# Optimization experiments

Hardware: AMD Instinct MI355X
Metric: run time of the kernel (lower is better)

## Reference

```python
import jax, jax.numpy as jnp
import numpy as np

B, M, T, D, V = 16, 1024, 4096, 512, 32000
HOPS = 2  # multi_layer_gcn layer_number=2


def setup_inputs() -> dict:
    key = jax.random.key(0)
    ks = jax.random.split(key, 10)
    s = 1.0 / np.sqrt(D)
    emb = jax.random.normal(ks[0], (V, D), jnp.float32) * 0.02
    Ws = jax.random.normal(ks[1], (HOPS, D, D), jnp.float32) * s
    Wn = jax.random.normal(ks[2], (HOPS, D, D), jnp.float32) * s
    Wr = jax.random.normal(ks[3], (HOPS, D, D), jnp.float32) * s
    Wt = jax.random.normal(ks[4], (D, 3 * D), jnp.float32) * (1.0 / np.sqrt(3 * D))
    concept_ids = jax.random.randint(ks[5], (B, M), 0, V)
    relation = jax.random.randint(ks[6], (B, T), 0, V)
    head = jax.random.randint(ks[7], (B, T), 0, M)
    tail = jax.random.randint(ks[8], (B, T), 0, M)
    triple_label = jax.random.randint(ks[9], (B, T), -1, 2)  # {-1,0,1}
    return dict(emb=emb, Ws=Ws, Wn=Wn, Wr=Wr, Wt=Wt,
                concept_ids=concept_ids, relation=relation,
                head=head, tail=tail, triple_label=triple_label)


def _forward(emb, Ws, Wn, Wr, Wt, concept_ids, relation, head, tail, triple_label):
    x = emb[concept_ids]        # [B, M, D] node hidden
    rel = emb[relation]         # [B, T, D] relation hidden
    mask = (triple_label != -1).astype(x.dtype)  # [B, T]

    # per-batch scatter_add into M node slots
    scat = jax.vmap(lambda msg, idx: jnp.zeros((M, msg.shape[-1]), msg.dtype).at[idx].add(msg))
    scat1 = jax.vmap(lambda v, idx: jnp.zeros((M,), v.dtype).at[idx].add(v))

    for i in range(HOPS):
        oh = jnp.take_along_axis(x, head[..., None], axis=1) * mask[..., None]  # gather heads
        ot = jnp.take_along_axis(x, tail[..., None], axis=1) * mask[..., None]  # gather tails
        relm = rel * mask[..., None]
        # update_node += scatter(head_repr - rel -> tail) + scatter(tail_repr - rel -> head)
        upd = scat(oh - relm, tail) + scat(ot - relm, head)          # [B, M, D]
        cnt = scat1(mask, tail) + scat1(mask, head)                  # [B, M]
        x = jax.nn.relu(
            jnp.einsum('bmd,ed->bme', x, Ws[i])
            + jnp.einsum('bmd,ed->bme', upd, Wn[i]) / jnp.maximum(cnt, 1.0)[..., None]
        )
        rel = jnp.einsum('btd,ed->bte', rel, Wr[i])

    head_repr = jnp.take_along_axis(x, head[..., None], axis=1)  # [B, T, D]
    tail_repr = jnp.take_along_axis(x, tail[..., None], axis=1)  # [B, T, D]
    triple_repr = jnp.concatenate([head_repr, rel, tail_repr], axis=-1)  # [B, T, 3D]
    triple_repr = jnp.einsum('btk,dk->btd', triple_repr, Wt)     # [B, T, D]
    encoded_cause = triple_repr.sum(axis=1)                      # [B, D]
    return triple_repr, encoded_cause


def reference(emb, Ws, Wn, Wr, Wt, concept_ids, relation, head, tail, triple_label):
    return _forward(emb, Ws, Wn, Wr, Wt, concept_ids, relation, head, tail, triple_label)
```

## Files before the change

kernel.cpp:

```cpp
#include <hip/hip_runtime.h>

namespace {

constexpr int kB = 16;
constexpr int kM = 1024;
constexpr int kT = 4096;
constexpr int kD = 512;
constexpr int kV = 32000;

typedef __attribute__((ext_vector_type(8))) short bfrag8;
typedef __attribute__((ext_vector_type(4))) float f4acc;

__device__ __forceinline__ ushort f2bf(float f) {
  unsigned u = __float_as_uint(f);
  u += 0x7fffu + ((u >> 16) & 1u);
  return (ushort)(u >> 16);
}
__device__ __forceinline__ float bf2f(ushort h) {
  return __uint_as_float(((unsigned)h) << 16);
}

__device__ __forceinline__ void gload_lds16(const void* g, void* l) {
  __builtin_amdgcn_global_load_lds(
      (const __attribute__((address_space(1))) void*)g,
      (__attribute__((address_space(3))) void*)l, 16, 0, 0);
}

constexpr int kN0 = kV * kD / 4;
constexpr int kN1 = kN0 + 2 * kD * kD / 4;
constexpr int kN2 = kN1 + 2 * kD * kD / 4;
constexpr int kN3 = kN2 + kD * 1536 / 4;
constexpr int kN4 = kN3 + kB * kM * 128;
constexpr int kPREPB = kN4 / 8192;
constexpr int kCSRB = 16;
constexpr int kMM2B = 256;

__global__ __launch_bounds__(512) void fused_prep_k(
    const float4* __restrict__ emb, const float4* __restrict__ Ws,
    const float4* __restrict__ Wn, const float4* __restrict__ Wt,
    const float* __restrict__ Wnf, const float* __restrict__ Wtf,
    const float* __restrict__ Wrf,
    const int* __restrict__ cid,
    const int* __restrict__ headp, const int* __restrict__ tailp,
    const int* __restrict__ lblp,
    ushort4* __restrict__ EMBb, ushort4* __restrict__ Wsb,
    ushort4* __restrict__ Wnb, ushort4* __restrict__ Wtb,
    ushort4* __restrict__ X0,
    int* __restrict__ deg, int* __restrict__ rowstart, int* __restrict__ epack,
    ushort* __restrict__ Wn2r, float* __restrict__ T1)
{
  __shared__ __align__(16) char shm[45056];
  const int bid = blockIdx.x;
  const int tid = threadIdx.x;

  if (bid < kCSRB) {
    int* sdeg = (int*)shm;
    int* sscan = (int*)(shm + 4096);
    int* sfill = (int*)(shm + 8192);
    int* sep = (int*)(shm + 12288);
    const int b = bid;
    const int n0 = tid, n1 = tid + 512;
    sdeg[n0] = 0; sdeg[n1] = 0;
    __syncthreads();
    const int* hb = headp + (b << 12);
    const int* tb = tailp + (b << 12);
    const int* lb = lblp + (b << 12);
    for (int t = tid; t < kT; t += 512) {
      if (lb[t] == -1) continue;
      atomicAdd(&sdeg[tb[t]], 1);
      atomicAdd(&sdeg[hb[t]], 1);
    }
    __syncthreads();
    int d0 = sdeg[n0], d1 = sdeg[n1];
    sscan[n0] = d0; sscan[n1] = d1;
    __syncthreads();
    for (int off = 1; off < kM; off <<= 1) {
      int v0 = (n0 >= off) ? sscan[n0 - off] : 0;
      int v1 = (n1 >= off) ? sscan[n1 - off] : 0;
      __syncthreads();
      sscan[n0] += v0; sscan[n1] += v1;
      __syncthreads();
    }
    int lrs0 = sscan[n0] - d0;
    int lrs1 = sscan[n1] - d1;
    deg[(b << 10) + n0] = d0;
    deg[(b << 10) + n1] = d1;
    rowstart[(b << 10) + n0] = b * (2 * kT) + lrs0;
    rowstart[(b << 10) + n1] = b * (2 * kT) + lrs1;
    sfill[n0] = lrs0; sfill[n1] = lrs1;
    __syncthreads();
    for (int t = tid; t < kT; t += 512) {
      if (lb[t] == -1) continue;
      int hd = hb[t];
      int tl = tb[t];
      int p0 = atomicAdd(&sfill[tl], 1);
      sep[p0] = ((t * 2) << 10) | hd;
      int p1 = atomicAdd(&sfill[hd], 1);
      sep[p1] = ((t * 2 + 1) << 10) | tl;
    }
    __syncthreads();
#pragma unroll
    for (int nn = 0; nn < 2; ++nn) {
      int lrs = nn ? lrs1 : lrs0;
      int d = nn ? d1 : d0;
      for (int i = 1; i < d; ++i) {
        int key = sep[lrs + i];
        int j = i - 1;
        while (j >= 0 && sep[lrs + j] > key) {
          sep[lrs + j + 1] = sep[lrs + j];
          --j;
        }
        sep[lrs + j + 1] = key;
      }
    }
    __syncthreads();
    for (int i = tid; i < 2 * kT; i += 512)
      epack[b * (2 * kT) + i] = sep[i];
  } else if (bid < kCSRB + kPREPB) {
    const int bidp = bid - kCSRB;
    for (int c = 0; c < 4; ++c) {
      const int base = (bidp * 4 + c) * 2048 + tid;
      const float4* sp[4];
      ushort4* dp[4];
#pragma unroll
      for (int j = 0; j < 4; ++j) {
        int i = base + j * 512;
        if (i < kN0) { sp[j] = emb + i; dp[j] = EMBb + i; }
        else if (i < kN1) { sp[j] = Ws + (i - kN0); dp[j] = Wsb + (i - kN0); }
        else if (i < kN2) { sp[j] = Wn + (i - kN1); dp[j] = Wnb + (i - kN1); }
        else if (i < kN3) { sp[j] = Wt + (i - kN2); dp[j] = Wtb + (i - kN2); }
        else {
          int idx = i - kN3;
          sp[j] = emb + (size_t)cid[idx >> 7] * 128 + (idx & 127);
          dp[j] = X0 + idx;
        }
      }
      float4 v[4];
#pragma unroll
      for (int j = 0; j < 4; ++j) v[j] = *sp[j];
#pragma unroll
      for (int j = 0; j < 4; ++j) {
        ushort4 o;
        o.x = f2bf(v[j].x); o.y = f2bf(v[j].y);
        o.z = f2bf(v[j].z); o.w = f2bf(v[j].w);
        *dp[j] = o;
      }
    }
  } else {
    float (*prow)[512] = (float(*)[512])shm;
    const int mb = bid - kCSRB - kPREPB;
    const int job = mb >> 7;
    const int e0 = (mb & 127) * 4;
    const int k = tid;
    const float* P;
    int strideP, offsP;
    const float* Q;
    if (job == 0) { P = Wnf + (size_t)kD * kD; strideP = 512; offsP = 0; Q = Wrf; }
    else { P = Wtf; strideP = 1536; offsP = 512; Q = Wrf + (size_t)kD * kD; }
#pragma unroll
    for (int i = 0; i < 4; ++i)
      prow[i][k] = P[(size_t)(e0 + i) * strideP + offsP + k];
    __syncthreads();
    float acc[4] = {0.f, 0.f, 0.f, 0.f};
    for (int a = 0; a < 512; a += 8) {
      float qv[8];
#pragma unroll
      for (int u = 0; u < 8; ++u) qv[u] = Q[(a + u) * 512 + k];
#pragma unroll
      for (int u = 0; u < 8; ++u)
#pragma unroll
        for (int i = 0; i < 4; ++i)
          acc[i] = fmaf(prow[i][a + u], qv[u], acc[i]);
    }
#pragma unroll
    for (int i = 0; i < 4; ++i) {
      if (job == 0) Wn2r[(e0 + i) * 512 + k] = f2bf(acc[i]);
      else T1[(e0 + i) * 512 + k] = acc[i];
    }
  }
}

constexpr int kFOLDB = 128;

__global__ __launch_bounds__(512) void fold_aggxr_k(
    const float* __restrict__ T1, const float* __restrict__ Wrf,
    ushort* __restrict__ Wfold,
    const ushort4* __restrict__ Xv, const ushort4* __restrict__ EMBv,
    const int* __restrict__ relid,
    const int* __restrict__ deg, const int* __restrict__ rowstart,
    const int* __restrict__ epack,
    ushort4* __restrict__ SxC, ushort4* __restrict__ nSr0n)
{
  __shared__ float prow[4][512];
  const int bid = blockIdx.x;
  const int tid = threadIdx.x;
  if (bid < kFOLDB) {
    int e0 = bid * 4;
    int k = tid;
#pragma unroll
    for (int i = 0; i < 4; ++i)
      prow[i][k] = T1[(size_t)(e0 + i) * 512 + k];
    __syncthreads();
    float acc[4] = {0.f, 0.f, 0.f, 0.f};
    for (int a = 0; a < 512; a += 8) {
      float qv[8];
#pragma unroll
      for (int u = 0; u < 8; ++u) qv[u] = Wrf[(a + u) * 512 + k];
#pragma unroll
      for (int u = 0; u < 8; ++u)
#pragma unroll
        for (int i = 0; i < 4; ++i)
          acc[i] = fmaf(prow[i][a + u], qv[u], acc[i]);
    }
#pragma unroll
    for (int i = 0; i < 4; ++i) Wfold[(e0 + i) * 512 + k] = f2bf(acc[i]);
  } else {
    int bm = (bid - kFOLDB) * 4 + (tid >> 7);
    int t128 = tid & 127;
    int b = bm >> 10;
    int dg = deg[bm];
    int rs = rowstart[bm];
    const int* rid = relid + (b << 12);
    size_t xbase = (size_t)b * kM * 128;
    float ax = 0.f, ay = 0.f, az = 0.f, aw = 0.f;
    float rx = 0.f, ry = 0.f, rz = 0.f, rw = 0.f;
    int e = 0;
    for (; e + 4 <= dg; e += 4) {
      int pk[4];
#pragma unroll
      for (int j = 0; j < 4; ++j) pk[j] = epack[rs + e + j];
      ushort4 xv[4], rv[4];
#pragma unroll
      for (int j = 0; j < 4; ++j) {
        xv[j] = Xv[xbase + (size_t)(pk[j] & 1023) * 128 + t128];
        rv[j] = EMBv[(size_t)rid[pk[j] >> 11] * 128 + t128];
      }
#pragma unroll
      for (int j = 0; j < 4; ++j) {
        ax += bf2f(xv[j].x); ay += bf2f(xv[j].y);
        az += bf2f(xv[j].z); aw += bf2f(xv[j].w);
        rx += bf2f(rv[j].x); ry += bf2f(rv[j].y);
        rz += bf2f(rv[j].z); rw += bf2f(rv[j].w);
      }
    }
    for (; e < dg; ++e) {
      int pk = epack[rs + e];
      ushort4 xv = Xv[xbase + (size_t)(pk & 1023) * 128 + t128];
      ushort4 rv = EMBv[(size_t)rid[pk >> 11] * 128 + t128];
      ax += bf2f(xv.x); ay += bf2f(xv.y); az += bf2f(xv.z); aw += bf2f(xv.w);
      rx += bf2f(rv.x); ry += bf2f(rv.y); rz += bf2f(rv.z); rw += bf2f(rv.w);
    }
    float s = 1.0f / (float)(dg > 0 ? dg : 1);
    ushort4 o;
    o.x = f2bf((ax - rx) * s); o.y = f2bf((ay - ry) * s);
    o.z = f2bf((az - rz) * s); o.w = f2bf((aw - rw) * s);
    SxC[(size_t)bm * 128 + t128] = o;
    o.x = f2bf(-rx * s); o.y = f2bf(-ry * s);
    o.z = f2bf(-rz * s); o.w = f2bf(-rw * s);
    nSr0n[(size_t)bm * 128 + t128] = o;
  }
}

__global__ __launch_bounds__(128) void agg_x_k(
    const ushort4* __restrict__ Xv,
    const int* __restrict__ deg, const int* __restrict__ rowstart,
    const int* __restrict__ epack, ushort4* __restrict__ outv)
{
  int bm = blockIdx.x;
  int b = bm >> 10;
  int tid = threadIdx.x;
  int dg = deg[bm];
  int rs = rowstart[bm];
  size_t xbase = (size_t)b * kM * 128;
  float ax = 0.f, ay = 0.f, az = 0.f, aw = 0.f;
  int e = 0;
  for (; e + 4 <= dg; e += 4) {
    int pk[4];
#pragma unroll
    for (int j = 0; j < 4; ++j) pk[j] = epack[rs + e + j];
    ushort4 xv[4];
#pragma unroll
    for (int j = 0; j < 4; ++j)
      xv[j] = Xv[xbase + (size_t)(pk[j] & 1023) * 128 + tid];
#pragma unroll
    for (int j = 0; j < 4; ++j) {
      ax += bf2f(xv[j].x); ay += bf2f(xv[j].y);
      az += bf2f(xv[j].z); aw += bf2f(xv[j].w);
    }
  }
  for (; e < dg; ++e) {
    int src = epack[rs + e] & 1023;
    ushort4 xv = Xv[xbase + (size_t)src * 128 + tid];
    ax += bf2f(xv.x); ay += bf2f(xv.y); az += bf2f(xv.z); aw += bf2f(xv.w);
  }
  float s = 1.0f / (float)(dg > 0 ? dg : 1);
  ushort4 o;
  o.x = f2bf(ax * s); o.y = f2bf(ay * s); o.z = f2bf(az * s); o.w = f2bf(aw * s);
  outv[(size_t)bm * 128 + tid] = o;
}

template<int MODE>
__global__ __launch_bounds__(256) void gemm_k(
    const ushort* __restrict__ A0, const ushort* __restrict__ A1,
    const ushort* __restrict__ A2,
    const ushort* __restrict__ W1, const ushort* __restrict__ W2,
    const ushort* __restrict__ W3,
    ushort* __restrict__ outbf)
{
  constexpr int NSEG = (MODE == 0) ? 3 : (MODE == 1) ? 2 : 1;
  constexpr bool RELU = (MODE == 0) || (MODE == 1);
  constexpr int NC = (MODE == 4) ? 8 : 4;
  constexpr int OSTR = (MODE == 4) ? 1024 : 512;
  constexpr bool SWZ = (MODE != 5);

  __shared__ __align__(16) char lds[32768];
  char* ldsA = lds;
  char* ldsB = lds + 16384;
  const int tid = threadIdx.x;
  const int w = tid >> 6;
  const int l = tid & 63;
  const int wr = w >> 1;
  const int wc = w & 1;
  const int bid = blockIdx.x;
  int panel, col;
  if constexpr (SWZ) {
    int xcd = bid & 7;
    int idx = bid >> 3;
    panel = xcd * (((int)gridDim.x >> 3) / NC) + idx / NC;
    col = idx % NC;
  } else {
    panel = bid >> 2;
    col = bid & 3;
  }
  const int rowBase = panel * 128;
  const int colBase = col * 128;

  f4acc acc[4][4];
#pragma unroll
  for (int i = 0; i < 4; ++i)
#pragma unroll
    for (int j = 0; j < 4; ++j) acc[i][j] = (f4acc)(0.f);

  int lrow[4], gc[4];
#pragma unroll
  for (int i = 0; i < 4; ++i) {
    int P = (i * 4 + w) * 64 + l;
    lrow[i] = P >> 3;
    gc[i] = (P & 7) ^ (lrow[i] & 7);
  }

  for (int seg = 0; seg < NSEG; ++seg) {
    const char* aP[4];
    const char* bP[4];
#pragma unroll
    for (int i = 0; i < 4; ++i) {
      int grow = rowBase + lrow[i];
      const ushort* ab;
      if constexpr (MODE == 0) {
        ab = (seg == 0 ? A0 : (seg == 1 ? A1 : A2)) + (size_t)grow * kD;
      } else if constexpr (MODE == 1) {
        ab = (seg == 0 ? A0 : A1) + (size_t)grow * kD;
      } else {
        ab = A0 + (size_t)grow * kD;
      }
      aP[i] = (const char*)ab + gc[i] * 16;
      int e = colBase + lrow[i];
      const ushort* wb;
      if constexpr (MODE == 0) {
        wb = (seg == 0 ? W1 : (seg == 1 ? W2 : W3)) + (size_t)e * kD;
      } else if constexpr (MODE == 1) {
        wb = (seg == 0 ? W1 : W2) + (size_t)e * kD;
      } else if constexpr (MODE == 4) {
        wb = W1 + (size_t)(e & 511) * 1536 + (e >> 9) * 1024;
      } else {
        wb = W1 + (size_t)e * kD;
      }
      bP[i] = (const char*)wb + gc[i] * 16;
    }
    for (int kcl = 0; kcl < 8; ++kcl) {
      __syncthreads();
#pragma unroll
      for (int i = 0; i < 4; ++i) {
        gload_lds16(aP[i] + kcl * 128, ldsA + (i * 4 + w) * 1024);
        gload_lds16(bP[i] + kcl * 128, ldsB + (i * 4 + w) * 1024);
      }
      __syncthreads();
#pragma unroll
      for (int ksub = 0; ksub < 2; ++ksub) {
        bfrag8 ef[4], wf[4];
#pragma unroll
        for (int mi = 0; mi < 4; ++mi) {
          int r = wr * 64 + mi * 16 + (l & 15);
          int g = (ksub * 4 + (l >> 4)) ^ (r & 7);
          ef[mi] = *(const bfrag8*)(ldsA + r * 128 + g * 16);
        }
#pragma unroll
        for (int ni = 0; ni < 4; ++ni) {
          int e = wc * 64 + ni * 16 + (l & 15);
          int g = (ksub * 4 + (l >> 4)) ^ (e & 7);
          wf[ni] = *(const bfrag8*)(ldsB + e * 128 + g * 16);
        }
#pragma unroll
        for (int mi = 0; mi < 4; ++mi)
#pragma unroll
          for (int ni = 0; ni < 4; ++ni)
            acc[mi][ni] = __builtin_amdgcn_mfma_f32_16x16x32_bf16(
                wf[ni], ef[mi], acc[mi][ni], 0, 0, 0);
      }
    }
  }

#pragma unroll
  for (int mi = 0; mi < 4; ++mi) {
    int rr = rowBase + wr * 64 + mi * 16 + (l & 15);
#pragma unroll
    for (int ni = 0; ni < 4; ++ni) {
      int cc0 = colBase + wc * 64 + ni * 16 + (l >> 4) * 4;
      float v0 = acc[mi][ni][0], v1 = acc[mi][ni][1];
      float v2 = acc[mi][ni][2], v3 = acc[mi][ni][3];
      if constexpr (RELU) {
        v0 = fmaxf(v0, 0.f); v1 = fmaxf(v1, 0.f);
        v2 = fmaxf(v2, 0.f); v3 = fmaxf(v3, 0.f);
      }
      ushort4 o;
      o.x = f2bf(v0); o.y = f2bf(v1); o.z = f2bf(v2); o.w = f2bf(v3);
      *(ushort4*)(outbf + (size_t)rr * OSTR + cc0) = o;
    }
  }
}

__global__ __launch_bounds__(128) void final_add_k(
    const ushort4* __restrict__ REL2v, const ushort4* __restrict__ HTv,
    const int* __restrict__ relid, const int* __restrict__ headp,
    const int* __restrict__ tailp,
    float* __restrict__ outf, float* __restrict__ part)
{
  const int blk = blockIdx.x;
  const int tid = threadIdx.x;
  const int r0 = blk * 32;
  float cs0 = 0.f, cs1 = 0.f, cs2 = 0.f, cs3 = 0.f;
  for (int i = 0; i < 32; i += 8) {
    ushort4 rv[8], hv[8], tv[8];
#pragma unroll
    for (int j = 0; j < 8; ++j) {
      int r = r0 + i + j;
      int bb = r >> 12;
      rv[j] = REL2v[(size_t)relid[r] * 128 + tid];
      hv[j] = HTv[((size_t)(bb << 10) + headp[r]) * 256 + tid];
      tv[j] = HTv[((size_t)(bb << 10) + tailp[r]) * 256 + 128 + tid];
    }
#pragma unroll
    for (int j = 0; j < 8; ++j) {
      f4acc ov;
      ov[0] = bf2f(rv[j].x) + bf2f(hv[j].x) + bf2f(tv[j].x);
      ov[1] = bf2f(rv[j].y) + bf2f(hv[j].y) + bf2f(tv[j].y);
      ov[2] = bf2f(rv[j].z) + bf2f(hv[j].z) + bf2f(tv[j].z);
      ov[3] = bf2f(rv[j].w) + bf2f(hv[j].w) + bf2f(tv[j].w);
      cs0 += ov[0]; cs1 += ov[1]; cs2 += ov[2]; cs3 += ov[3];
      __builtin_nontemporal_store(
          ov, (f4acc*)(outf + (size_t)(r0 + i + j) * 512 + tid * 4));
    }
  }
  float4 o; o.x = cs0; o.y = cs1; o.z = cs2; o.w = cs3;
  *(float4*)(part + (size_t)blk * 512 + tid * 4) = o;
}

__global__ __launch_bounds__(512) void reduce_enc_k(
    const float* __restrict__ part, float* __restrict__ enc)
{
  int b = blockIdx.x;
  int c = threadIdx.x;
  float s = 0.f;
  for (int rt = 0; rt < 128; ++rt) s += part[(size_t)(b * 128 + rt) * 512 + c];
  enc[b * 512 + c] = s;
}

}

extern "C" void kernel_launch(void* const* d_in, const int* in_sizes, int n_in,
                              void* d_out, int out_size, void* d_ws, size_t ws_size,
                              hipStream_t stream) {
  const float* emb = (const float*)d_in[0];
  const float* Ws = (const float*)d_in[1];
  const float* Wn = (const float*)d_in[2];
  const float* Wr = (const float*)d_in[3];
  const float* Wt = (const float*)d_in[4];
  const int* cid = (const int*)d_in[5];
  const int* relid = (const int*)d_in[6];
  const int* headp = (const int*)d_in[7];
  const int* tailp = (const int*)d_in[8];
  const int* lblp = (const int*)d_in[9];
  float* out = (float*)d_out;

  char* wsp = (char*)d_ws;
  ushort* EMBb  = (ushort*)(wsp);
  ushort* HT    = (ushort*)(wsp);
  ushort* REL2  = (ushort*)(wsp + (32ull << 20));
  ushort* Wsb   = (ushort*)(wsp + (64ull << 20));
  ushort* Wnb   = (ushort*)(wsp + (65ull << 20));
  ushort* Wtb   = (ushort*)(wsp + (66ull << 20));
  ushort* Wn2r  = (ushort*)(wsp + (67ull << 20) + (512ull << 10));
  ushort* Wfold = (ushort*)(wsp + (68ull << 20));
  float*  T1    = (float*)(wsp + (68ull << 20) + (512ull << 10));
  int* deg      = (int*)(wsp + (70ull << 20));
  int* rowstart = deg + kB * kM;
  int* epack    = rowstart + kB * kM;
  float* part   = (float*)(wsp + (71ull << 20));

  char* outc = (char*)d_out;
  ushort* X0    = (ushort*)(outc);
  ushort* Sxn   = (ushort*)(outc + (16ull << 20));
  ushort* nSr0n = (ushort*)(outc + (32ull << 20));
  ushort* X1    = (ushort*)(outc + (48ull << 20));
  ushort* X2    = X0;
  float* ENC = out + (size_t)kB * kT * kD;

  fused_prep_k<<<kCSRB + kPREPB + kMM2B, 512, 0, stream>>>(
      (const float4*)emb, (const float4*)Ws, (const float4*)Wn,
      (const float4*)Wt, Wn, Wt, Wr, cid, headp, tailp, lblp,
      (ushort4*)EMBb, (ushort4*)Wsb, (ushort4*)Wnb, (ushort4*)Wtb,
      (ushort4*)X0, deg, rowstart, epack, Wn2r, T1);

  fold_aggxr_k<<<kFOLDB + kB * kM / 4, 512, 0, stream>>>(
      T1, Wr, Wfold, (const ushort4*)X0, (const ushort4*)EMBb, relid,
      deg, rowstart, epack, (ushort4*)Sxn, (ushort4*)nSr0n);

  gemm_k<1><<<(kB * kM / 128) * 4, 256, 0, stream>>>(
      X0, Sxn, nullptr, Wsb, Wnb, nullptr, X1);

  gemm_k<5><<<(kV / 128) * 4, 256, 0, stream>>>(
      EMBb, nullptr, nullptr, Wfold, nullptr, nullptr, REL2);

  agg_x_k<<<kB * kM, 128, 0, stream>>>(
      (const ushort4*)X1, deg, rowstart, epack, (ushort4*)Sxn);

  gemm_k<0><<<(kB * kM / 128) * 4, 256, 0, stream>>>(
      X1, Sxn, nSr0n, Wsb + (size_t)kD * kD, Wnb + (size_t)kD * kD, Wn2r, X2);

  gemm_k<4><<<(kB * kM / 128) * 8, 256, 0, stream>>>(
      X2, nullptr, nullptr, Wtb, nullptr, nullptr, HT);

  final_add_k<<<kB * kT / 32, 128, 0, stream>>>(
      (const ushort4*)REL2, (const ushort4*)HT, relid, headp, tailp, out, part);

  reduce_enc_k<<<kB, 512, 0, stream>>>(part, ENC);
}
```

Before: 261.4 us.

## Split per-batch CSR build into parallel count, scan, fill and sort kernels

Replaces the 16-block in-LDS CSR construction (degree count, scan, fill, insertion sort), which ran inside the prep kernel, with a pipeline. Degree counting now uses global atomics spread over 128 blocks, followed by separate scan, fill and per-row sort kernels. The aim is to stop 16 long-running blocks from serialising the prep kernel's tail. In exchange it adds a memset, three extra launches, and global-memory atomics and sorting in place of LDS.

```diff
diff --git a/kernel.cpp b/kernel.cpp
--- a/kernel.cpp
+++ b/kernel.cpp
@@ -31,8 +31,8 @@
 constexpr int kN2 = kN1 + 2 * kD * kD / 4;
 constexpr int kN3 = kN2 + kD * 1536 / 4;
 constexpr int kN4 = kN3 + kB * kM * 128;
+constexpr int kCNTB = 128;
 constexpr int kPREPB = kN4 / 8192;
-constexpr int kCSRB = 16;
 constexpr int kMM2B = 256;
 
 __global__ __launch_bounds__(512) void fused_prep_k(
@@ -46,78 +46,22 @@
     ushort4* __restrict__ EMBb, ushort4* __restrict__ Wsb,
     ushort4* __restrict__ Wnb, ushort4* __restrict__ Wtb,
     ushort4* __restrict__ X0,
-    int* __restrict__ deg, int* __restrict__ rowstart, int* __restrict__ epack,
+    int* __restrict__ deg,
     ushort* __restrict__ Wn2r, float* __restrict__ T1)
 {
-  __shared__ __align__(16) char shm[45056];
+  __shared__ __align__(16) float prow[4][512];
   const int bid = blockIdx.x;
   const int tid = threadIdx.x;
 
-  if (bid < kCSRB) {
-    int* sdeg = (int*)shm;
-    int* sscan = (int*)(shm + 4096);
-    int* sfill = (int*)(shm + 8192);
-    int* sep = (int*)(shm + 12288);
-    const int b = bid;
-    const int n0 = tid, n1 = tid + 512;
-    sdeg[n0] = 0; sdeg[n1] = 0;
-    __syncthreads();
-    const int* hb = headp + (b << 12);
-    const int* tb = tailp + (b << 12);
-    const int* lb = lblp + (b << 12);
-    for (int t = tid; t < kT; t += 512) {
-      if (lb[t] == -1) continue;
-      atomicAdd(&sdeg[tb[t]], 1);
-      atomicAdd(&sdeg[hb[t]], 1);
-    }
-    __syncthreads();
-    int d0 = sdeg[n0], d1 = sdeg[n1];
-    sscan[n0] = d0; sscan[n1] = d1;
-    __syncthreads();
-    for (int off = 1; off < kM; off <<= 1) {
-      int v0 = (n0 >= off) ? sscan[n0 - off] : 0;
-      int v1 = (n1 >= off) ? sscan[n1 - off] : 0;
-      __syncthreads();
-      sscan[n0] += v0; sscan[n1] += v1;
-      __syncthreads();
-    }
-    int lrs0 = sscan[n0] - d0;
-    int lrs1 = sscan[n1] - d1;
-    deg[(b << 10) + n0] = d0;
-    deg[(b << 10) + n1] = d1;
-    rowstart[(b << 10) + n0] = b * (2 * kT) + lrs0;
-    rowstart[(b << 10) + n1] = b * (2 * kT) + lrs1;
-    sfill[n0] = lrs0; sfill[n1] = lrs1;
-    __syncthreads();
-    for (int t = tid; t < kT; t += 512) {
-      if (lb[t] == -1) continue;
-      int hd = hb[t];
-      int tl = tb[t];
-      int p0 = atomicAdd(&sfill[tl], 1);
-      sep[p0] = ((t * 2) << 10) | hd;
-      int p1 = atomicAdd(&sfill[hd], 1);
-      sep[p1] = ((t * 2 + 1) << 10) | tl;
-    }
-    __syncthreads();
-#pragma unroll
-    for (int nn = 0; nn < 2; ++nn) {
-      int lrs = nn ? lrs1 : lrs0;
-      int d = nn ? d1 : d0;
-      for (int i = 1; i < d; ++i) {
-        int key = sep[lrs + i];
-        int j = i - 1;
-        while (j >= 0 && sep[lrs + j] > key) {
-          sep[lrs + j + 1] = sep[lrs + j];
-          --j;
-        }
-        sep[lrs + j + 1] = key;
-      }
-    }
-    __syncthreads();
-    for (int i = tid; i < 2 * kT; i += 512)
-      epack[b * (2 * kT) + i] = sep[i];
-  } else if (bid < kCSRB + kPREPB) {
-    const int bidp = bid - kCSRB;
+  if (bid < kCNTB) {
+    int i = bid * 512 + tid;
+    if (lblp[i] != -1) {
+      int b = i >> 12;
+      atomicAdd(&deg[(b << 10) + tailp[i]], 1);
+      atomicAdd(&deg[(b << 10) + headp[i]], 1);
+    }
+  } else if (bid < kCNTB + kPREPB) {
+    const int bidp = bid - kCNTB;
     for (int c = 0; c < 4; ++c) {
       const int base = (bidp * 4 + c) * 2048 + tid;
       const float4* sp[4];
@@ -147,8 +91,7 @@
       }
     }
   } else {
-    float (*prow)[512] = (float(*)[512])shm;
-    const int mb = bid - kCSRB - kPREPB;
+    const int mb = bid - kCNTB - kPREPB;
     const int job = mb >> 7;
     const int e0 = (mb & 127) * 4;
     const int k = tid;
@@ -177,6 +120,64 @@
       if (job == 0) Wn2r[(e0 + i) * 512 + k] = f2bf(acc[i]);
       else T1[(e0 + i) * 512 + k] = acc[i];
     }
+  }
+}
+
+__global__ __launch_bounds__(1024) void scan_k(
+    const int* __restrict__ deg, int* __restrict__ rowstart,
+    int* __restrict__ fillptr)
+{
+  __shared__ int s[kM];
+  int b = blockIdx.x;
+  int tid = threadIdx.x;
+  int d = deg[b * kM + tid];
+  s[tid] = d;
+  __syncthreads();
+  for (int off = 1; off < kM; off <<= 1) {
+    int add = (tid >= off) ? s[tid - off] : 0;
+    __syncthreads();
+    s[tid] += add;
+    __syncthreads();
+  }
+  int rs = b * (2 * kT) + s[tid] - d;
+  rowstart[b * kM + tid] = rs;
+  fillptr[b * kM + tid] = rs;
+}
+
+__global__ __launch_bounds__(256) void fill_k(
+    const int* __restrict__ headp, const int* __restrict__ tailp,
+    const int* __restrict__ lblp, int* __restrict__ fillptr,
+    int* __restrict__ epack)
+{
+  int i = blockIdx.x * 256 + threadIdx.x;
+  if (i >= kB * kT) return;
+  if (lblp[i] == -1) return;
+  int b = i >> 12;
+  int t = i & (kT - 1);
+  int hd = headp[i];
+  int tl = tailp[i];
+  int p0 = atomicAdd(&fillptr[(b << 10) + tl], 1);
+  epack[p0] = ((t * 2) << 10) | hd;
+  int p1 = atomicAdd(&fillptr[(b << 10) + hd], 1);
+  epack[p1] = ((t * 2 + 1) << 10) | tl;
+}
+
+__global__ __launch_bounds__(256) void sort_k(
+    const int* __restrict__ rowstart, const int* __restrict__ deg,
+    int* __restrict__ epack)
+{
+  int bm = blockIdx.x * 256 + threadIdx.x;
+  if (bm >= kB * kM) return;
+  int rs = rowstart[bm];
+  int dg = deg[bm];
+  for (int i = 1; i < dg; ++i) {
+    int key = epack[rs + i];
+    int j = i - 1;
+    while (j >= 0 && epack[rs + j] > key) {
+      epack[rs + j + 1] = epack[rs + j];
+      --j;
+    }
+    epack[rs + j + 1] = key;
   }
 }
 
@@ -504,7 +505,8 @@
   float*  T1    = (float*)(wsp + (68ull << 20) + (512ull << 10));
   int* deg      = (int*)(wsp + (70ull << 20));
   int* rowstart = deg + kB * kM;
-  int* epack    = rowstart + kB * kM;
+  int* fillptr  = rowstart + kB * kM;
+  int* epack    = fillptr + kB * kM;
   float* part   = (float*)(wsp + (71ull << 20));
 
   char* outc = (char*)d_out;
@@ -515,11 +517,18 @@
   ushort* X2    = X0;
   float* ENC = out + (size_t)kB * kT * kD;
 
-  fused_prep_k<<<kCSRB + kPREPB + kMM2B, 512, 0, stream>>>(
+  hipMemsetAsync(deg, 0, (size_t)kB * kM * sizeof(int), stream);
+
+  fused_prep_k<<<kCNTB + kPREPB + kMM2B, 512, 0, stream>>>(
       (const float4*)emb, (const float4*)Ws, (const float4*)Wn,
       (const float4*)Wt, Wn, Wt, Wr, cid, headp, tailp, lblp,
       (ushort4*)EMBb, (ushort4*)Wsb, (ushort4*)Wnb, (ushort4*)Wtb,
-      (ushort4*)X0, deg, rowstart, epack, Wn2r, T1);
+      (ushort4*)X0, deg, Wn2r, T1);
+
+  scan_k<<<kB, 1024, 0, stream>>>(deg, rowstart, fillptr);
+  fill_k<<<(kB * kT + 255) / 256, 256, 0, stream>>>(
+      headp, tailp, lblp, fillptr, epack);
+  sort_k<<<(kB * kM + 255) / 256, 256, 0, stream>>>(rowstart, deg, epack);
 
   fold_aggxr_k<<<kFOLDB + kB * kM / 4, 512, 0, stream>>>(
       T1, Wr, Wfold, (const ushort4*)X0, (const ushort4*)EMBb, relid,
```

Result: slower. 294.8 us (+12.8%).
